# Kernel optimization log

Measured on AMD Instinct MI355X. Metric: run time of the kernel, lower is better.

The kernel has to match this reference:

```python
import jax, jax.numpy as jnp
import numpy as np

B, S, E, H = 4, 1024, 1024, 16
D = E // H  # 64


def setup_inputs() -> dict:
    key = jax.random.key(0)
    ks = jax.random.split(key, 11)
    scale = 1.0 / np.sqrt(E)
    inp = {
        "q": jax.random.normal(ks[0], (B, S, E), jnp.float32),
        "k": jax.random.normal(ks[1], (B, S, E), jnp.float32),
        "v": jax.random.normal(ks[2], (B, S, E), jnp.float32),
        "mask": jax.random.randint(ks[3], (B, 1, 1, S), 0, 2, jnp.int32),
        # torch.nn.Linear params: W is [out, in], y = x @ W.T + b
        "Wq": jax.random.uniform(ks[4], (E, E), jnp.float32, -scale, scale),
        "bq": jax.random.uniform(ks[5], (E,), jnp.float32, -scale, scale),
        "Wk": jax.random.uniform(ks[6], (E, E), jnp.float32, -scale, scale),
        "bk": jax.random.uniform(ks[7], (E,), jnp.float32, -scale, scale),
        "Wo": jax.random.uniform(ks[8], (E, E), jnp.float32, -scale, scale),
        "bo": jax.random.uniform(ks[9], (E,), jnp.float32, -scale, scale),
    }
    return inp


def reference(q, k, v, mask, Wq, bq, Wk, bk, Wo, bo):
    # Projections. NOTE: original code applies key_linear to v (value_linear unused).
    qh = (q @ Wq.T + bq).reshape(B, S, H, D).transpose(0, 2, 1, 3)  # [B,H,S,D]
    kh = (k @ Wk.T + bk).reshape(B, S, H, D).transpose(0, 2, 1, 3)
    vh = (v @ Wk.T + bk).reshape(B, S, H, D).transpose(0, 2, 1, 3)

    scores = jnp.einsum("bhqd,bhkd->bhqk", qh, kh) / jnp.sqrt(jnp.float32(D))
    pad = mask == 0  # [B,1,1,S] broadcast
    scores = jnp.where(pad, jnp.float32(-1e9), scores)
    attn = jax.nn.softmax(scores, axis=-1)
    attn = jnp.where(pad, jnp.float32(0.0), attn)

    ctx = jnp.einsum("bhqk,bhkd->bhqd", attn, vh)  # [B,H,S,D]
    ctx = ctx.transpose(0, 2, 1, 3).reshape(B, S, E)
    return ctx @ Wo.T + bo
```

## Files before the change

kernel.cpp:

```cpp
#include <hip/hip_runtime.h>

typedef unsigned short u16;
typedef unsigned int   u32;
typedef __attribute__((ext_vector_type(8))) short bf16x8;
typedef __attribute__((ext_vector_type(4))) float f32x4;
typedef __attribute__((ext_vector_type(4))) u32   u32x4;

#define MFMA(a,b,c) __builtin_amdgcn_mfma_f32_16x16x32_bf16(a,b,c,0,0,0)


__device__ __forceinline__ u32 cvtpk(float lo, float hi){
  u32 r; asm("v_cvt_pk_bf16_f32 %0, %1, %2" : "=v"(r) : "v"(lo), "v"(hi)); return r;
}
__device__ __forceinline__ u16 f2bf(float f){ return (u16)cvtpk(f,f); }
__device__ __forceinline__ bf16x8 cvt8(f32x4 lo, f32x4 hi){
  u32x4 u;
  u.x = cvtpk(lo[0],lo[1]); u.y = cvtpk(lo[2],lo[3]);
  u.z = cvtpk(hi[0],hi[1]); u.w = cvtpk(hi[2],hi[3]);
  return *(bf16x8*)&u;
}

__device__ __forceinline__ int swz(int row, int col){
  return (((row<<6) + col)<<1) ^ ((row&7)<<4);
}

__device__ __forceinline__ void gl16(const void* g, void* l){
  __builtin_amdgcn_global_load_lds(
      (const __attribute__((address_space(1))) u32*)g,
      (__attribute__((address_space(3))) u32*)l, 16, 0, 0);
}

template<int ROWS>
__device__ __forceinline__ void stage_bf16(const u16* g, size_t ldg, char* lds, int wv, int lane){
  #pragma unroll
  for (int i=0;i<ROWS/32;++i){
    const int r0 = wv*(ROWS/4) + (i<<3);
    const int row = r0 + (lane>>3);
    const int c = ((lane&7) ^ (row&7)) << 3;
    gl16(g + (size_t)row*ldg + c, lds + (r0<<7));
  }
}

__device__ __forceinline__ bf16x8 frag_bf16(const char* lds, int row, int kcol){
  return *(const bf16x8*)(lds + swz(row,kcol));
}

__global__ __launch_bounds__(256) void prep_k(
    const float* __restrict__ wq, const float* __restrict__ wk, const float* __restrict__ wo,
    const float* __restrict__ q,  const float* __restrict__ k,  const float* __restrict__ v,
    u16* __restrict__ out,
    const int* __restrict__ mask, int* __restrict__ gidx, int* __restrict__ cnts)
{
  const int tid = threadIdx.x;
  if (blockIdx.x < 7680){
    const size_t i8 = (((size_t)blockIdx.x<<8) + tid) << 3;
    const float* src;
    if      (i8 <  1048576u) src = wq + i8;
    else if (i8 <  2097152u) src = wk + (i8 - 1048576u);
    else if (i8 <  3145728u) src = wo + (i8 - 2097152u);
    else if (i8 <  7340032u) src = q  + (i8 - 3145728u);
    else if (i8 < 11534336u) src = k  + (i8 - 7340032u);
    else                     src = v  + (i8 - 11534336u);
    f32x4 lo = *(const f32x4*)src, hi = *(const f32x4*)(src+4);
    *(bf16x8*)(out + i8) = cvt8(lo, hi);
  } else {
    const int b = blockIdx.x - 7680, lane = tid&63, wv = tid>>6;
    __shared__ int wsum[4];
    int4 z4; z4.x=0; z4.y=0; z4.z=0; z4.w=0;
    *(int4*)(gidx + (b<<10) + (tid<<2)) = z4;
    const int4 m = *(const int4*)(mask + (b<<10) + (tid<<2));
    const int c0 = (m.x!=0)+(m.y!=0)+(m.z!=0)+(m.w!=0);
    int pre = c0;
    #pragma unroll
    for (int i=1;i<64;i<<=1){
      int t = __shfl_up(pre, i);
      if (lane >= i) pre += t;
    }
    if (lane==63) wsum[wv] = pre;
    __syncthreads();
    int base = pre - c0;
    #pragma unroll
    for (int w=0;w<4;++w) if (w<wv) base += wsum[w];
    int p = base;
    const int s0 = tid<<2;
    if (m.x) gidx[(b<<10) + p++] = s0;
    if (m.y) gidx[(b<<10) + p++] = s0+1;
    if (m.z) gidx[(b<<10) + p++] = s0+2;
    if (m.w) gidx[(b<<10) + p++] = s0+3;
    if (tid==255) cnts[b] = p;
  }
}

template<int V, bool GA, bool GB>
__device__ __forceinline__ void proj_body(
    const u16* __restrict__ Aa, const u16* __restrict__ Bb,
    const int* __restrict__ gA, const int* __restrict__ gB,
    const float* __restrict__ bias, u16* __restrict__ outb,
    char* As, char* Bs)
{
  const int tid = threadIdx.x, lane = tid&63, wv = tid>>6;
  const int wm = wv>>1, wn = wv&1, l15 = lane&15, g4 = lane>>4;

  int growA[4], growB[4];
  if (GA){
    #pragma unroll
    for (int i=0;i<4;++i) growA[i] = gA[(wv<<5)+(i<<3)+(lane>>3)] & 1023;
  }
  if (GB){
    #pragma unroll
    for (int i=0;i<4;++i) growB[i] = gB[(wv<<5)+(i<<3)+(lane>>3)] & 1023;
  }

  f32x4 acc[4][4] = {};

  #pragma unroll 1
  for (int kt=0; kt<1024; kt+=64){
    __syncthreads();
    #pragma unroll
    for (int i=0;i<4;++i){
      const int r0 = (wv<<5)+(i<<3), row = r0+(lane>>3);
      const int c = ((lane&7)^(row&7))<<3;
      const u16* srcA = GA ? Aa + (size_t)growA[i]*1024 + kt + c
                           : Aa + (size_t)row*1024 + kt + c;
      gl16(srcA, As + (r0<<7));
      const u16* srcB = GB ? Bb + (size_t)growB[i]*1024 + kt + c
                           : Bb + (size_t)row*1024 + kt + c;
      gl16(srcB, Bs + (r0<<7));
    }
    __syncthreads();

    #pragma unroll
    for (int kb=0;kb<64;kb+=32){
      const int kcol = kb + (g4<<3);
      bf16x8 af[4], bf_[4];
      #pragma unroll
      for (int t=0;t<4;++t)
        af[t] = frag_bf16(As, (wm<<6) + (t<<4) + l15, kcol);
      #pragma unroll
      for (int t=0;t<4;++t)
        bf_[t] = frag_bf16(Bs, (wn<<6) + (t<<4) + l15, kcol);
      #pragma unroll
      for (int mt=0;mt<4;++mt)
        #pragma unroll
        for (int nt=0;nt<4;++nt)
          acc[mt][nt] = MFMA(af[mt], bf_[nt], acc[mt][nt]);
    }
  }

  f32x4 bmv[4];
  if (V==1){
    #pragma unroll
    for (int mt=0;mt<4;++mt)
      bmv[mt] = *(const f32x4*)(bias + (wm<<6) + (mt<<4) + (g4<<2));
  }
  #pragma unroll
  for (int nt=0;nt<4;++nt){
    const int col = (wn<<6) + (nt<<4) + l15;
    const float bvn = (V==1) ? 0.f : bias[col];
    #pragma unroll
    for (int mt=0;mt<4;++mt){
      f32x4 a = acc[mt][nt];
      #pragma unroll
      for (int j=0;j<4;++j){
        const int ml = (wm<<6) + (mt<<4) + (g4<<2) + j;
        const float val = a[j] + ((V==1) ? bmv[mt][j] : bvn);
        if (V==1) outb[(size_t)ml*4096 + col] = f2bf(val);
        else      outb[(size_t)ml*1024 + col] = f2bf(val);
      }
    }
  }
}

__global__ __launch_bounds__(256,4) void proj_k(
    const u16* __restrict__ qb, const u16* __restrict__ kb, const u16* __restrict__ vb,
    const u16* __restrict__ wqb, const u16* __restrict__ wkb,
    const float* __restrict__ bq, const float* __restrict__ bk,
    u16* __restrict__ qp, u16* __restrict__ kp, u16* __restrict__ vt,
    const int* __restrict__ gidx, const int* __restrict__ cnts)
{
  __shared__ __align__(16) char As[16384];
  __shared__ __align__(16) char Bs[16384];
  const int bid = blockIdx.x;
  if (bid < 256){
    const int m0 = (bid&31)<<7, n0 = ((bid>>5)&7)<<7;
    proj_body<0,false,false>(qb + (size_t)m0*1024, wqb + (size_t)n0*1024, nullptr, nullptr,
                             bq + n0, qp + (size_t)m0*1024 + n0, As, Bs);
  } else if (bid < 512){
    const int local = bid-256;
    const int m0 = (local&31)<<7, n0 = ((local>>5)&7)<<7;
    const int b = m0>>10, mloc = m0&1023;
    if (mloc >= cnts[b]) return;
    proj_body<0,true,false>(kb + ((size_t)(b<<10))*1024, wkb + (size_t)n0*1024,
                            gidx + (b<<10) + mloc, nullptr,
                            bk + n0, kp + ((size_t)((b<<10)+mloc))*1024 + n0, As, Bs);
  } else {
    const int local = bid-512;
    const int m0 = (local&7)<<7, n0 = (local>>3)<<7;
    const int b = n0>>10, nloc = n0&1023;
    if (nloc >= cnts[b]) return;
    proj_body<1,false,true>(wkb + (size_t)m0*1024, vb + ((size_t)(b<<10))*1024,
                            nullptr, gidx + (b<<10) + nloc,
                            bk + m0, vt + (size_t)m0*4096 + (b<<10) + nloc, As, Bs);
  }
}

__global__ __launch_bounds__(256,4) void oproj_k(
    const u16* __restrict__ ctx, const u16* __restrict__ wob,
    const float* __restrict__ bo, float* __restrict__ of)
{
  constexpr int BN = 64, NT = 2;
  __shared__ __align__(16) char As[16384];
  __shared__ __align__(16) char Bs[BN*128];
  const int m0 = blockIdx.x<<7, n0 = blockIdx.y*BN;
  const int tid = threadIdx.x, lane = tid&63, wv = tid>>6;
  const int wm = wv>>1, wn = wv&1, l15 = lane&15, g4 = lane>>4;

  f32x4 acc[4][NT] = {};

  #pragma unroll 1
  for (int kt=0; kt<1024; kt+=64){
    __syncthreads();
    stage_bf16<128>(ctx + (size_t)m0*1024 + kt, 1024, As, wv, lane);
    stage_bf16<BN> (wob + (size_t)n0*1024 + kt, 1024, Bs, wv, lane);
    __syncthreads();

    #pragma unroll
    for (int kb=0;kb<64;kb+=32){
      const int kcol = kb + (g4<<3);
      bf16x8 af[4], bf_[NT];
      #pragma unroll
      for (int t=0;t<4;++t)
        af[t] = frag_bf16(As, (wm<<6) + (t<<4) + l15, kcol);
      #pragma unroll
      for (int t=0;t<NT;++t)
        bf_[t] = frag_bf16(Bs, wn*(BN>>1) + (t<<4) + l15, kcol);
      #pragma unroll
      for (int mt=0;mt<4;++mt)
        #pragma unroll
        for (int nt=0;nt<NT;++nt)
          acc[mt][nt] = MFMA(af[mt], bf_[nt], acc[mt][nt]);
    }
  }

  #pragma unroll
  for (int nt=0;nt<NT;++nt){
    const int col = n0 + wn*(BN>>1) + (nt<<4) + l15;
    const float bvn = bo[col];
    #pragma unroll
    for (int mt=0;mt<4;++mt){
      const int mb = m0 + (wm<<6) + (mt<<4) + (g4<<2);
      f32x4 a = acc[mt][nt];
      #pragma unroll
      for (int j=0;j<4;++j)
        of[(size_t)(mb+j)*1024 + col] = a[j] + bvn;
    }
  }
}

__global__ __launch_bounds__(256) void attn_k(
    const u16* __restrict__ qp, const u16* __restrict__ kp, const u16* __restrict__ vt,
    const int* __restrict__ cnts, u16* __restrict__ ctx)
{
  const int bid = blockIdx.x;
  const int wg  = (bid&7)*64 + (bid>>3);
  const int qt = wg&7, h = (wg>>3)&15, b = wg>>7;

  __shared__ __align__(16) u16 Qs[128*64];
  __shared__ __align__(16) u16 Ks[2][64*64];
  __shared__ __align__(16) u16 Vs[2][64*64];
  __shared__ __align__(16) u16 Ps[4*32*64];

  const int tid = threadIdx.x, lane = tid&63, wv = tid>>6;
  const int hc = h<<6, l15 = lane&15;
  const float C2 = 0.18033688011112042f;

  const int cnt = cnts[b];
  const int ntiles = (cnt + 63) >> 6;

  {
    const u16* Qg = qp + ((size_t)((b<<10) + (qt<<7)))*1024 + hc;
    #pragma unroll
    for (int i=0;i<4;++i){
      const int r0 = (wv<<5) + (i<<3);
      const int row = r0 + (lane>>3);
      const int c = ((lane&7) ^ (row&7)) << 3;
      gl16(Qg + (size_t)row*1024 + c, (char*)Qs + (r0<<7));
    }
  }

  const u16* Kg = kp + ((size_t)(b<<10))*1024 + hc;
  const u16* Vg = vt + ((size_t)hc)*4096 + (b<<10);

  auto stageKV = [&](int kt2, int bi){
    #pragma unroll
    for (int i=0;i<2;++i){
      const int r0 = (wv<<4) + (i<<3);
      const int row = r0 + (lane>>3);
      const int c = ((lane&7) ^ (row&7)) << 3;
      gl16(Kg + (size_t)((kt2<<6) + row)*1024 + c, (char*)Ks[bi] + (r0<<7));
      gl16(Vg + (size_t)row*4096 + (kt2<<6) + c,  (char*)Vs[bi] + (r0<<7));
    }
  };
  stageKV(0, 0);
  __syncthreads();

  f32x4 o[2][4] = {};
  float lr[2][4] = {};
  u16* Pw = Ps + (wv<<11);
  int cur = 0;

  #pragma unroll 1
  for (int kt=0; kt<ntiles; ++kt){
    if (kt+1 < ntiles) stageKV(kt+1, cur^1);
    const char* Kc = (const char*)Ks[cur];
    const char* Vc = (const char*)Vs[cur];

    f32x4 sc[2][4] = {};
    #pragma unroll
    for (int kb=0;kb<64;kb+=32){
      const int kcol = kb + ((lane>>4)<<3);
      bf16x8 kf[4];
      #pragma unroll
      for (int nt=0;nt<4;++nt) kf[nt] = frag_bf16(Kc, (nt<<4)+l15, kcol);
      bf16x8 aq0 = frag_bf16((const char*)Qs, (wv<<5)+l15, kcol);
      bf16x8 aq1 = frag_bf16((const char*)Qs, (wv<<5)+16+l15, kcol);
      __builtin_amdgcn_s_setprio(1);
      #pragma unroll
      for (int nt=0;nt<4;++nt) sc[0][nt] = MFMA(aq0, kf[nt], sc[0][nt]);
      #pragma unroll
      for (int nt=0;nt<4;++nt) sc[1][nt] = MFMA(aq1, kf[nt], sc[1][nt]);
      __builtin_amdgcn_s_setprio(0);
    }

    float bv4[4];
    #pragma unroll
    for (int nt=0;nt<4;++nt)
      bv4[nt] = ((kt<<6)+(nt<<4)+l15 < cnt) ? 0.f : -1e30f;
    #pragma unroll
    for (int sub=0;sub<2;++sub)
      #pragma unroll
      for (int nt=0;nt<4;++nt){
        f32x4 s = sc[sub][nt];
        #pragma unroll
        for (int j=0;j<4;++j){
          const float p = __builtin_amdgcn_exp2f(fmaf(s[j], C2, bv4[nt]));
          lr[sub][j] += p;
          *(u16*)((char*)Pw + swz((sub<<4)+((lane>>4)<<2)+j, (nt<<4)+l15)) = f2bf(p);
        }
      }
    asm volatile("s_waitcnt lgkmcnt(0)" ::: "memory");
    __builtin_amdgcn_sched_barrier(0);

    #pragma unroll
    for (int kb=0;kb<64;kb+=32){
      const int kcol = kb + ((lane>>4)<<3);
      bf16x8 vf[4];
      #pragma unroll
      for (int nt=0;nt<4;++nt) vf[nt] = frag_bf16(Vc, (nt<<4)+l15, kcol);
      bf16x8 pa0 = frag_bf16((const char*)Pw, l15, kcol);
      bf16x8 pa1 = frag_bf16((const char*)Pw, 16+l15, kcol);
      __builtin_amdgcn_s_setprio(1);
      #pragma unroll
      for (int nt=0;nt<4;++nt) o[0][nt] = MFMA(pa0, vf[nt], o[0][nt]);
      #pragma unroll
      for (int nt=0;nt<4;++nt) o[1][nt] = MFMA(pa1, vf[nt], o[1][nt]);
      __builtin_amdgcn_s_setprio(0);
    }
    __syncthreads();
    cur ^= 1;
  }

  #pragma unroll
  for (int sub=0;sub<2;++sub)
    #pragma unroll
    for (int j=0;j<4;++j){
      float s = lr[sub][j];
      s += __shfl_xor(s,1); s += __shfl_xor(s,2);
      s += __shfl_xor(s,4); s += __shfl_xor(s,8);
      const float inv = 1.f / fmaxf(s, 1e-30f);
      const int row = (qt<<7) + (wv<<5) + (sub<<4) + ((lane>>4)<<2) + j;
      u16* crow = ctx + ((size_t)((b<<10)+row))*1024 + hc;
      #pragma unroll
      for (int nt=0;nt<4;++nt)
        crow[(nt<<4)+l15] = f2bf(o[sub][nt][j]*inv);
    }
}

extern "C" void kernel_launch(void* const* d_in, const int* in_sizes, int n_in,
                              void* d_out, int out_size, void* d_ws, size_t ws_size,
                              hipStream_t stream) {
  const float* q    = (const float*)d_in[0];
  const float* k    = (const float*)d_in[1];
  const float* v    = (const float*)d_in[2];
  const int*   mask = (const int*)  d_in[3];
  const float* Wq   = (const float*)d_in[4];
  const float* bq   = (const float*)d_in[5];
  const float* Wk   = (const float*)d_in[6];
  const float* bk   = (const float*)d_in[7];
  const float* Wo   = (const float*)d_in[8];
  const float* bo   = (const float*)d_in[9];
  float* out = (float*)d_out;

  char* ws = (char*)d_ws;
  u16* wqb  = (u16*)(ws);
  u16* wkb  = (u16*)(ws +  2097152);
  u16* wob  = (u16*)(ws +  4194304);
  u16* qb   = (u16*)(ws +  6291456);
  u16* kb   = (u16*)(ws + 14680064);
  u16* vb   = (u16*)(ws + 23068672);
  u16* qp   = (u16*)(ws + 31457280);
  u16* kp   = (u16*)(ws + 39845888);
  u16* vtb  = (u16*)(ws + 48234496);
  u16* ctxb = (u16*)(ws + 56623104);
  int* gidx = (int*)(ws + 65011712);
  int* cnts = (int*)(ws + 65028096);

  dim3 blk(256);
  prep_k<<<7684, blk, 0, stream>>>(Wq, Wk, Wo, q, k, v, wqb, mask, gidx, cnts);
  proj_k<<<768, blk, 0, stream>>>(qb, kb, vb, wqb, wkb, bq, bk, qp, kp, vtb, gidx, cnts);
  attn_k<<<512, blk, 0, stream>>>(qp, kp, vtb, cnts, ctxb);
  oproj_k<<<dim3(32,16), blk, 0, stream>>>(ctxb, wob, bo, out);
}
```

Measured before the change: 84.54 us.

## Skip converting masked K/V rows and single-buffer K/V tiles in attention

The prep kernel now reads the mask and exits early for key and value rows whose mask is zero, so those rows are never converted from fp32 to bf16. This cuts read and write traffic in the conversion pass, on the assumption that later stages only use the compacted unmasked keys. Separately, the attention kernel drops double-buffered K/V staging for a single buffer loaded at the top of each tile between two barriers. That lowers LDS use per block, which may allow more resident blocks, but it gives up the overlap of the next tile's loads with the current tile's compute.

Result: faster. 81.51 us (median of 2 runs) (-3.6%).

```diff
diff --git a/kernel.cpp b/kernel.cpp
--- a/kernel.cpp
+++ b/kernel.cpp
@@ -59,8 +59,15 @@
     else if (i8 <  2097152u) src = wk + (i8 - 1048576u);
     else if (i8 <  3145728u) src = wo + (i8 - 2097152u);
     else if (i8 <  7340032u) src = q  + (i8 - 3145728u);
-    else if (i8 < 11534336u) src = k  + (i8 - 7340032u);
-    else                     src = v  + (i8 - 11534336u);
+    else if (i8 < 11534336u){
+      const size_t off = i8 - 7340032u;
+      if (!mask[off>>10]) return;
+      src = k + off;
+    } else {
+      const size_t off = i8 - 11534336u;
+      if (!mask[off>>10]) return;
+      src = v + off;
+    }
     f32x4 lo = *(const f32x4*)src, hi = *(const f32x4*)(src+4);
     *(bf16x8*)(out + i8) = cvt8(lo, hi);
   } else {
@@ -266,8 +273,8 @@
   const int qt = wg&7, h = (wg>>3)&15, b = wg>>7;
 
   __shared__ __align__(16) u16 Qs[128*64];
-  __shared__ __align__(16) u16 Ks[2][64*64];
-  __shared__ __align__(16) u16 Vs[2][64*64];
+  __shared__ __align__(16) u16 Ks[64*64];
+  __shared__ __align__(16) u16 Vs[64*64];
   __shared__ __align__(16) u16 Ps[4*32*64];
 
   const int tid = threadIdx.x, lane = tid&63, wv = tid>>6;
@@ -291,29 +298,24 @@
   const u16* Kg = kp + ((size_t)(b<<10))*1024 + hc;
   const u16* Vg = vt + ((size_t)hc)*4096 + (b<<10);
 
-  auto stageKV = [&](int kt2, int bi){
-    #pragma unroll
-    for (int i=0;i<2;++i){
-      const int r0 = (wv<<4) + (i<<3);
-      const int row = r0 + (lane>>3);
-      const int c = ((lane&7) ^ (row&7)) << 3;
-      gl16(Kg + (size_t)((kt2<<6) + row)*1024 + c, (char*)Ks[bi] + (r0<<7));
-      gl16(Vg + (size_t)row*4096 + (kt2<<6) + c,  (char*)Vs[bi] + (r0<<7));
-    }
-  };
-  stageKV(0, 0);
-  __syncthreads();
-
   f32x4 o[2][4] = {};
   float lr[2][4] = {};
   u16* Pw = Ps + (wv<<11);
-  int cur = 0;
 
   #pragma unroll 1
   for (int kt=0; kt<ntiles; ++kt){
-    if (kt+1 < ntiles) stageKV(kt+1, cur^1);
-    const char* Kc = (const char*)Ks[cur];
-    const char* Vc = (const char*)Vs[cur];
+    __syncthreads();
+    {
+      #pragma unroll
+      for (int i=0;i<2;++i){
+        const int r0 = (wv<<4) + (i<<3);
+        const int row = r0 + (lane>>3);
+        const int c = ((lane&7) ^ (row&7)) << 3;
+        gl16(Kg + (size_t)((kt<<6) + row)*1024 + c, (char*)Ks + (r0<<7));
+        gl16(Vg + (size_t)row*4096 + (kt<<6) + c,  (char*)Vs + (r0<<7));
+      }
+    }
+    __syncthreads();
 
     f32x4 sc[2][4] = {};
     #pragma unroll
@@ -321,7 +323,7 @@
       const int kcol = kb + ((lane>>4)<<3);
       bf16x8 kf[4];
       #pragma unroll
-      for (int nt=0;nt<4;++nt) kf[nt] = frag_bf16(Kc, (nt<<4)+l15, kcol);
+      for (int nt=0;nt<4;++nt) kf[nt] = frag_bf16((const char*)Ks, (nt<<4)+l15, kcol);
       bf16x8 aq0 = frag_bf16((const char*)Qs, (wv<<5)+l15, kcol);
       bf16x8 aq1 = frag_bf16((const char*)Qs, (wv<<5)+16+l15, kcol);
       __builtin_amdgcn_s_setprio(1);
@@ -356,7 +358,7 @@
       const int kcol = kb + ((lane>>4)<<3);
       bf16x8 vf[4];
       #pragma unroll
-      for (int nt=0;nt<4;++nt) vf[nt] = frag_bf16(Vc, (nt<<4)+l15, kcol);
+      for (int nt=0;nt<4;++nt) vf[nt] = frag_bf16((const char*)Vs, (nt<<4)+l15, kcol);
       bf16x8 pa0 = frag_bf16((const char*)Pw, l15, kcol);
       bf16x8 pa1 = frag_bf16((const char*)Pw, 16+l15, kcol);
       __builtin_amdgcn_s_setprio(1);
@@ -366,8 +368,6 @@
       for (int nt=0;nt<4;++nt) o[1][nt] = MFMA(pa1, vf[nt], o[1][nt]);
       __builtin_amdgcn_s_setprio(0);
     }
-    __syncthreads();
-    cur ^= 1;
   }
 
   #pragma unroll
```
